# Kernel optimization log

Measured on AMD Instinct MI355X. Metric: run time of the kernel, lower is better.

The kernel has to match this reference:

```python
import jax, jax.numpy as jnp
import numpy as np

B, N, D = 4, 1024, 1024
NH = 16
HS = D // NH
HID = 4 * D
EPS = 1e-5

def layernorm(x, w, b):
    mu = jnp.mean(x, axis=-1, keepdims=True)
    var = jnp.mean(jnp.square(x - mu), axis=-1, keepdims=True)
    return (x - mu) * jax.lax.rsqrt(var + EPS) * w + b

def setup_inputs() -> dict:
    key = jax.random.key(0)
    ks = jax.random.split(key, 8)
    s = lambda fan_in: 1.0 / np.sqrt(fan_in)
    return {
        "x": jax.random.normal(ks[0], (B, N, D), jnp.float32),
        "qkv_w": jax.random.uniform(ks[1], (3 * D, D), jnp.float32, -s(D), s(D)),
        "proj_w": jax.random.uniform(ks[2], (D, D), jnp.float32, -s(D), s(D)),
        "proj_b": jax.random.uniform(ks[3], (D,), jnp.float32, -s(D), s(D)),
        "ln1_w": jnp.ones((D,), jnp.float32),
        "ln1_b": jnp.zeros((D,), jnp.float32),
        "fc1_w": jax.random.uniform(ks[4], (HID, D), jnp.float32, -s(D), s(D)),
        "fc1_b": jax.random.uniform(ks[5], (HID,), jnp.float32, -s(D), s(D)),
        "fc2_w": jax.random.uniform(ks[6], (D, HID), jnp.float32, -s(HID), s(HID)),
        "fc2_b": jax.random.uniform(ks[7], (D,), jnp.float32, -s(HID), s(HID)),
        "ln2_w": jnp.ones((D,), jnp.float32),
        "ln2_b": jnp.zeros((D,), jnp.float32),
    }

def attention(x, qkv_w, proj_w, proj_b):
    # x: [b, n, d]; qkv linear (no bias), split into q,k,v per head
    qkv = jnp.einsum('bnd,ed->bne', x, qkv_w)              # [b, n, 3d]
    qkv = qkv.reshape(B, N, 3, NH, HS).transpose(2, 0, 3, 1, 4)  # [3, b, nh, n, hs]
    q, k, v = qkv[0], qkv[1], qkv[2]
    scale = HS ** -0.5
    # mask=False => self.mask == 1, so (mask-1)*LARGE_NUMBER == 0
    att = jax.nn.softmax(scale * jnp.einsum('bhqe,bhke->bhqk', q, k), axis=-1)
    y = jnp.einsum('bhqk,bhke->bhqe', att, v)              # [b, nh, n, hs]
    y = y.transpose(0, 2, 1, 3).reshape(B, N, D)
    return jnp.einsum('bnd,ed->bne', y, proj_w) + proj_b

def mlp(x, fc1_w, fc1_b, fc2_w, fc2_b):
    h = jax.nn.gelu(jnp.einsum('bnd,hd->bnh', x, fc1_w) + fc1_b, approximate=False)
    return jnp.einsum('bnh,dh->bnd', h, fc2_w) + fc2_b

def reference(x, qkv_w, proj_w, proj_b, ln1_w, ln1_b, fc1_w, fc1_b, fc2_w, fc2_b, ln2_w, ln2_b):
    x = x + attention(layernorm(x, ln1_w, ln1_b), qkv_w, proj_w, proj_b)
    x = x + mlp(layernorm(x, ln2_w, ln2_b), fc1_w, fc1_b, fc2_w, fc2_b)
    return x
```

## Files before the change

### kernel.cpp

```cpp
#include <hip/hip_runtime.h>
#include <hip/hip_bf16.h>

typedef __attribute__((ext_vector_type(8))) short short8;
typedef __attribute__((ext_vector_type(8))) unsigned short ushort8;
typedef __attribute__((ext_vector_type(4))) float floatx4;

#define DEV static __device__ __forceinline__

DEV unsigned short f2bf(float f) {
  unsigned int u = __builtin_bit_cast(unsigned int, f);
  u += 0x7fff + ((u >> 16) & 1);
  return (unsigned short)(u >> 16);
}
DEV float bf2f(unsigned short u) {
  return __builtin_bit_cast(float, (unsigned int)u << 16);
}
DEV unsigned int cvtpk_bf16(float lo, float hi) {
  unsigned int r;
  asm("v_cvt_pk_bf16_f32 %0, %1, %2" : "=v"(r) : "v"(lo), "v"(hi));
  return r;
}

DEV void gload_lds16(const void* g, void* l) {
  __builtin_amdgcn_global_load_lds(
      (const __attribute__((address_space(1))) unsigned int*)g,
      (__attribute__((address_space(3))) unsigned int*)l, 16, 0, 0);
}

__global__ __launch_bounds__(256) void cvt4_kernel(const float* __restrict__ w0,
                                                   const float* __restrict__ w1,
                                                   const float* __restrict__ w2,
                                                   const float* __restrict__ w3,
                                                   unsigned short* __restrict__ o0,
                                                   unsigned short* __restrict__ o1,
                                                   unsigned short* __restrict__ o2,
                                                   unsigned short* __restrict__ o3) {
  int i = blockIdx.x * 256 + threadIdx.x;
  const float* in; unsigned short* out; int j;
  if (i < 786432)       { in = w0; out = o0; j = i; }
  else if (i < 1048576) { in = w1; out = o1; j = i - 786432; }
  else if (i < 2097152) { in = w2; out = o2; j = i - 1048576; }
  else                  { in = w3; out = o3; j = i - 2097152; }
  float4 v = reinterpret_cast<const float4*>(in)[j];
  ushort4 o;
  o.x = f2bf(v.x); o.y = f2bf(v.y); o.z = f2bf(v.z); o.w = f2bf(v.w);
  reinterpret_cast<ushort4*>(out)[j] = o;
}

__global__ __launch_bounds__(256) void ln_kernel(const float* __restrict__ x,
                                                 const float* __restrict__ w,
                                                 const float* __restrict__ b,
                                                 unsigned short* __restrict__ out) {
  const int row = blockIdx.x;
  const float* xr = x + (size_t)row * 1024;
  float4 v = reinterpret_cast<const float4*>(xr)[threadIdx.x];
  float s  = v.x + v.y + v.z + v.w;
  float ss = v.x*v.x + v.y*v.y + v.z*v.z + v.w*v.w;
  #pragma unroll
  for (int off = 1; off < 64; off <<= 1) {
    s  += __shfl_xor(s, off);
    ss += __shfl_xor(ss, off);
  }
  __shared__ float red[8];
  const int wid = threadIdx.x >> 6, lane = threadIdx.x & 63;
  if (lane == 0) { red[wid] = s; red[4 + wid] = ss; }
  __syncthreads();
  s  = red[0] + red[1] + red[2] + red[3];
  ss = red[4] + red[5] + red[6] + red[7];
  const float mu  = s * (1.0f / 1024.0f);
  const float var = ss * (1.0f / 1024.0f) - mu * mu;
  const float rstd = rsqrtf(var + 1e-5f);
  float4 wv = reinterpret_cast<const float4*>(w)[threadIdx.x];
  float4 bv = reinterpret_cast<const float4*>(b)[threadIdx.x];
  ushort4 o;
  o.x = f2bf((v.x - mu) * rstd * wv.x + bv.x);
  o.y = f2bf((v.y - mu) * rstd * wv.y + bv.y);
  o.z = f2bf((v.z - mu) * rstd * wv.z + bv.z);
  o.w = f2bf((v.w - mu) * rstd * wv.w + bv.w);
  reinterpret_cast<ushort4*>(out)[(size_t)row * 256 + threadIdx.x] = o;
}

template<int EPI>
__global__ __launch_bounds__(512, 2) void gemm256(const unsigned short* __restrict__ A,
                                                  const unsigned short* __restrict__ Bw,
                                                  unsigned short* __restrict__ outb,
                                                  const float* __restrict__ bias,
                                                  int K, int N, int NT) {
  __shared__ unsigned short As[2][256 * 64];
  __shared__ unsigned short Bs[2][256 * 64];
  const int tid = threadIdx.x, lane = tid & 63, wid = tid >> 6;
  const int wr = wid >> 2, wc = wid & 3;
  const int fr = lane & 15, s0 = lane >> 4;

  const int nwg = gridDim.x;
  const int qq = nwg >> 3, rr8 = nwg & 7, xcd = blockIdx.x & 7, lid = blockIdx.x >> 3;
  const int wg = (xcd < rr8 ? xcd * (qq + 1) : rr8 * (qq + 1) + (xcd - rr8) * qq) + lid;
  const int brow = (wg / NT) * 256, bcol = (wg % NT) * 256;

  const unsigned short* ag[4];
  const unsigned short* bg[4];
  #pragma unroll
  for (int L = 0; L < 4; L++) {
    const int idx = L * 512 + tid;
    const int row = idx >> 3;
    const int ss  = ((idx & 7) ^ (row & 7)) * 8;
    ag[L] = A  + (size_t)(brow + row) * K + ss;
    bg[L] = Bw + (size_t)(bcol + row) * K + ss;
  }
  const int ldst = tid * 8;

  #define STG256(kt, buf)                                                     \
    do {                                                                      \
      const int ko = (kt) * 64;                                               \
      gload_lds16(ag[0] + ko, &As[buf][ldst]);                                \
      gload_lds16(ag[1] + ko, &As[buf][4096 + ldst]);                         \
      gload_lds16(ag[2] + ko, &As[buf][8192 + ldst]);                         \
      gload_lds16(ag[3] + ko, &As[buf][12288 + ldst]);                        \
      gload_lds16(bg[0] + ko, &Bs[buf][ldst]);                                \
      gload_lds16(bg[1] + ko, &Bs[buf][4096 + ldst]);                         \
      gload_lds16(bg[2] + ko, &Bs[buf][8192 + ldst]);                         \
      gload_lds16(bg[3] + ko, &Bs[buf][12288 + ldst]);                        \
    } while (0)

  const int xs = fr & 7;
  const int aoff = (wr * 128 + fr) * 64;
  const int boff = (wc * 64 + fr) * 64;
  const int sl0 = ((0 + s0) ^ xs) * 8;
  const int sl1 = ((4 + s0) ^ xs) * 8;

  floatx4 acc[8][4];
  #pragma unroll
  for (int m = 0; m < 8; m++)
    #pragma unroll
    for (int n = 0; n < 4; n++) acc[m][n] = (floatx4){0.f, 0.f, 0.f, 0.f};

  const int NTK = K >> 6;
  STG256(0, 0);

  for (int kt = 0; kt < NTK; ++kt) {
    const int cur = kt & 1;
    asm volatile("s_waitcnt vmcnt(0)" ::: "memory");
    __builtin_amdgcn_s_barrier();
    if (kt + 1 < NTK) STG256(kt + 1, cur ^ 1);

    const unsigned short* Ac = As[cur];
    const unsigned short* Bc = Bs[cur];
    short8 bfv[4][2], a0[4][2], a1[4][2];

    #pragma unroll
    for (int n = 0; n < 4; n++) {
      bfv[n][0] = *reinterpret_cast<const short8*>(Bc + boff + n * 1024 + sl0);
      bfv[n][1] = *reinterpret_cast<const short8*>(Bc + boff + n * 1024 + sl1);
    }
    #pragma unroll
    for (int m = 0; m < 4; m++) {
      a0[m][0] = *reinterpret_cast<const short8*>(Ac + aoff + m * 1024 + sl0);
      a0[m][1] = *reinterpret_cast<const short8*>(Ac + aoff + m * 1024 + sl1);
    }
    __builtin_amdgcn_s_setprio(1);
    #pragma unroll
    for (int m = 0; m < 4; m++)
      #pragma unroll
      for (int n = 0; n < 4; n++) {
        acc[m][n] = __builtin_amdgcn_mfma_f32_16x16x32_bf16(a0[m][0], bfv[n][0], acc[m][n], 0, 0, 0);
        acc[m][n] = __builtin_amdgcn_mfma_f32_16x16x32_bf16(a0[m][1], bfv[n][1], acc[m][n], 0, 0, 0);
      }
    __builtin_amdgcn_s_setprio(0);
    #pragma unroll
    for (int m = 0; m < 4; m++) {
      a1[m][0] = *reinterpret_cast<const short8*>(Ac + aoff + (m + 4) * 1024 + sl0);
      a1[m][1] = *reinterpret_cast<const short8*>(Ac + aoff + (m + 4) * 1024 + sl1);
    }
    __builtin_amdgcn_s_setprio(1);
    #pragma unroll
    for (int m = 0; m < 4; m++)
      #pragma unroll
      for (int n = 0; n < 4; n++) {
        acc[m + 4][n] = __builtin_amdgcn_mfma_f32_16x16x32_bf16(a1[m][0], bfv[n][0], acc[m + 4][n], 0, 0, 0);
        acc[m + 4][n] = __builtin_amdgcn_mfma_f32_16x16x32_bf16(a1[m][1], bfv[n][1], acc[m + 4][n], 0, 0, 0);
      }
    __builtin_amdgcn_s_setprio(0);
  }
  #undef STG256

  #pragma unroll
  for (int m = 0; m < 8; m++) {
    #pragma unroll
    for (int n = 0; n < 4; n++) {
      const int col = bcol + wc * 64 + n * 16 + fr;
      #pragma unroll
      for (int r = 0; r < 4; r++) {
        const size_t idx = (size_t)(brow + wr * 128 + m * 16 + s0 * 4 + r) * N + col;
        float v = acc[m][n][r];
        if (EPI == 1) {
          v += bias[col];
          const float u = v * 0.7978845608f * (1.0f + 0.044715f * v * v);
          const float e = __expf(2.0f * u);
          v = v * (e / (e + 1.0f));
        }
        outb[idx] = f2bf(v);
      }
    }
  }
}

__global__ __launch_bounds__(512) void gemm128sk(const unsigned short* __restrict__ A,
                                                 const unsigned short* __restrict__ Bw,
                                                 unsigned short* __restrict__ outb,
                                                 int K, int Ksl, int N, int NT, int ntiles) {
  __shared__ unsigned short As[4][128 * 32];
  __shared__ unsigned short Bs[4][128 * 32];
  const int tid = threadIdx.x, lane = tid & 63, wid = tid >> 6;
  const int wrow = (wid >> 2) * 64, wcol = (wid & 3) * 32;
  const int fr = lane & 15, s0 = lane >> 4;

  const int nwg = gridDim.x;
  const int qq = nwg >> 3, rr8 = nwg & 7, xcd = blockIdx.x & 7, lid = blockIdx.x >> 3;
  const int wg = (xcd < rr8 ? xcd * (qq + 1) : rr8 * (qq + 1) + (xcd - rr8) * qq) + lid;
  const int kslice = wg / ntiles, t = wg % ntiles;
  const int brow = (t / NT) * 128, bcol = (t % NT) * 128;
  const int kofs = kslice * Ksl;

  const int srow = tid >> 2;
  const int sslot = ((tid & 3) ^ ((srow >> 1) & 3)) * 8;
  const unsigned short* ag = A  + (size_t)(brow + srow) * K + kofs + sslot;
  const unsigned short* bg = Bw + (size_t)(bcol + srow) * K + kofs + sslot;
  const int ldst = tid * 8;

  #define STG(kt, buf)                              \
    do {                                            \
      const int ko = (kt) * 32;                     \
      gload_lds16(ag + ko, &As[buf][ldst]);         \
      gload_lds16(bg + ko, &Bs[buf][ldst]);         \
    } while (0)

  const int slr = (s0 ^ ((fr >> 1) & 3)) * 8;

  floatx4 acc[4][2];
  #pragma unroll
  for (int i = 0; i < 4; i++)
    #pragma unroll
    for (int j = 0; j < 2; j++) acc[i][j] = (floatx4){0.f, 0.f, 0.f, 0.f};

  const int NTK = Ksl >> 5;
  STG(0, 0);
  STG(1, 1);
  STG(2, 2);

  for (int kt = 0; kt < NTK; ++kt) {
    const int cur = kt & 3;
    if (kt < NTK - 2) {
      asm volatile("s_waitcnt vmcnt(4)" ::: "memory");
    } else if (kt == NTK - 2) {
      asm volatile("s_waitcnt vmcnt(2)" ::: "memory");
    } else {
      asm volatile("s_waitcnt vmcnt(0)" ::: "memory");
    }
    __builtin_amdgcn_s_barrier();
    if (kt + 3 < NTK) STG(kt + 3, (kt + 3) & 3);

    short8 af[4], bf[2];
    #pragma unroll
    for (int i = 0; i < 4; i++)
      af[i] = *reinterpret_cast<const short8*>(&As[cur][(wrow + i * 16 + fr) * 32 + slr]);
    #pragma unroll
    for (int j = 0; j < 2; j++)
      bf[j] = *reinterpret_cast<const short8*>(&Bs[cur][(wcol + j * 16 + fr) * 32 + slr]);
    __builtin_amdgcn_s_setprio(1);
    #pragma unroll
    for (int i = 0; i < 4; i++)
      #pragma unroll
      for (int j = 0; j < 2; j++)
        acc[i][j] = __builtin_amdgcn_mfma_f32_16x16x32_bf16(af[i], bf[j], acc[i][j], 0, 0, 0);
    __builtin_amdgcn_s_setprio(0);
  }
  #undef STG

  unsigned short* po = outb + (size_t)kslice * ((size_t)ntiles * 16384);
  const int erow = brow + wrow + (s0 << 2);
  const int ecol = bcol + wcol + fr;
  #pragma unroll
  for (int i = 0; i < 4; i++)
    #pragma unroll
    for (int j = 0; j < 2; j++)
      #pragma unroll
      for (int r = 0; r < 4; r++)
        po[(size_t)(erow + i * 16 + r) * N + ecol + j * 16] = f2bf(acc[i][j][r]);
}

__global__ __launch_bounds__(256) void red_ln(const unsigned short* __restrict__ p0,
                                              const unsigned short* __restrict__ p1,
                                              const float* __restrict__ x,
                                              const float* __restrict__ bias,
                                              const float* __restrict__ lw,
                                              const float* __restrict__ lb,
                                              float* __restrict__ x1,
                                              unsigned short* __restrict__ xn) {
  const int row = blockIdx.x, t = threadIdx.x;
  const size_t o4 = (size_t)row * 256 + t;
  ushort4 a = reinterpret_cast<const ushort4*>(p0)[o4];
  ushort4 c = reinterpret_cast<const ushort4*>(p1)[o4];
  float4 xv = reinterpret_cast<const float4*>(x)[o4];
  float4 bv = reinterpret_cast<const float4*>(bias)[t];
  float4 v;
  v.x = bf2f(a.x) + bf2f(c.x) + bv.x + xv.x;
  v.y = bf2f(a.y) + bf2f(c.y) + bv.y + xv.y;
  v.z = bf2f(a.z) + bf2f(c.z) + bv.z + xv.z;
  v.w = bf2f(a.w) + bf2f(c.w) + bv.w + xv.w;
  reinterpret_cast<float4*>(x1)[o4] = v;

  float s  = v.x + v.y + v.z + v.w;
  float ss = v.x*v.x + v.y*v.y + v.z*v.z + v.w*v.w;
  #pragma unroll
  for (int off = 1; off < 64; off <<= 1) {
    s  += __shfl_xor(s, off);
    ss += __shfl_xor(ss, off);
  }
  __shared__ float red[8];
  const int wid = t >> 6, lane = t & 63;
  if (lane == 0) { red[wid] = s; red[4 + wid] = ss; }
  __syncthreads();
  s  = red[0] + red[1] + red[2] + red[3];
  ss = red[4] + red[5] + red[6] + red[7];
  const float mu  = s * (1.0f / 1024.0f);
  const float var = ss * (1.0f / 1024.0f) - mu * mu;
  const float rstd = rsqrtf(var + 1e-5f);
  float4 wv = reinterpret_cast<const float4*>(lw)[t];
  float4 lv = reinterpret_cast<const float4*>(lb)[t];
  ushort4 o;
  o.x = f2bf((v.x - mu) * rstd * wv.x + lv.x);
  o.y = f2bf((v.y - mu) * rstd * wv.y + lv.y);
  o.z = f2bf((v.z - mu) * rstd * wv.z + lv.z);
  o.w = f2bf((v.w - mu) * rstd * wv.w + lv.w);
  reinterpret_cast<ushort4*>(xn)[o4] = o;
}

__global__ __launch_bounds__(256) void red_out(const unsigned short* __restrict__ p0,
                                               const unsigned short* __restrict__ p1,
                                               const float* __restrict__ x1,
                                               const float* __restrict__ bias,
                                               float* __restrict__ out) {
  const size_t i4 = (size_t)blockIdx.x * 256 + threadIdx.x;
  const int c4 = (int)(i4 & 255);
  ushort4 a = reinterpret_cast<const ushort4*>(p0)[i4];
  ushort4 c = reinterpret_cast<const ushort4*>(p1)[i4];
  float4 xv = reinterpret_cast<const float4*>(x1)[i4];
  float4 bv = reinterpret_cast<const float4*>(bias)[c4];
  float4 v;
  v.x = bf2f(a.x) + bf2f(c.x) + bv.x + xv.x;
  v.y = bf2f(a.y) + bf2f(c.y) + bv.y + xv.y;
  v.z = bf2f(a.z) + bf2f(c.z) + bv.z + xv.z;
  v.w = bf2f(a.w) + bf2f(c.w) + bv.w + xv.w;
  reinterpret_cast<float4*>(out)[i4] = v;
}

__global__ __launch_bounds__(256) void vtrans_kernel(const unsigned short* __restrict__ qkv,
                                                     unsigned short* __restrict__ vt) {
  __shared__ unsigned short T[64][66];
  const int nt = blockIdx.x, bh = blockIdx.y;
  const int b = bh >> 4, h = bh & 15;
  const unsigned short* src = qkv + (size_t)b * 1024 * 3072 + 2048 + h * 64;
  const int r = threadIdx.x >> 3, s = threadIdx.x & 7;
  ushort8 a0 = *reinterpret_cast<const ushort8*>(src + (size_t)(nt * 64 + r) * 3072 + s * 8);
  ushort8 a1 = *reinterpret_cast<const ushort8*>(src + (size_t)(nt * 64 + r + 32) * 3072 + s * 8);
  #pragma unroll
  for (int j = 0; j < 8; j++) {
    T[r][s * 8 + j]      = a0[j];
    T[r + 32][s * 8 + j] = a1[j];
  }
  __syncthreads();
  ushort8 o0, o1;
  #pragma unroll
  for (int j = 0; j < 8; j++) {
    o0[j] = T[s * 8 + j][r];
    o1[j] = T[s * 8 + j][r + 32];
  }
  unsigned short* dst = vt + (size_t)bh * 64 * 1024 + nt * 64 + s * 8;
  *reinterpret_cast<ushort8*>(dst + (size_t)r * 1024)        = o0;
  *reinterpret_cast<ushort8*>(dst + (size_t)(r + 32) * 1024) = o1;
}

__global__ __launch_bounds__(512) void attn_kernel(const unsigned short* __restrict__ qkv,
                                                   const unsigned short* __restrict__ vt,
                                                   unsigned short* __restrict__ y) {
  __shared__ unsigned short Ks[2][64 * 64];
  __shared__ unsigned short Vs[2][64 * 64];
  __shared__ unsigned long long Pq[8][256];

  const int tid = threadIdx.x;
  const int lane = tid & 63;
  const int w = tid >> 6;
  const int wg = (blockIdx.x & 7) * 64 + (blockIdx.x >> 3);
  const int bh = wg >> 3, qt = wg & 7;
  const int b = bh >> 4, h = bh & 15;
  const int fr = lane & 15, s0 = lane >> 4;
  const int sw = fr & 7;
  const size_t RS = 3072;

  const unsigned short* qbase = qkv + (size_t)b * 1024 * RS + h * 64;
  const unsigned short* kbase = qbase + 1024;
  const unsigned short* vbase = vt + (size_t)bh * 64 * 1024;

  const float SC = 0.125f * 1.44269504089f;

  short8 aq[2];
  {
    const unsigned short* qrow = qbase + (size_t)(qt * 128 + w * 16 + fr) * RS;
    ushort8 q0 = *reinterpret_cast<const ushort8*>(qrow + s0 * 8);
    ushort8 q1 = *reinterpret_cast<const ushort8*>(qrow + 32 + s0 * 8);
    #pragma unroll
    for (int i = 0; i < 8; i++) {
      q0[i] = f2bf(bf2f(q0[i]) * SC);
      q1[i] = f2bf(bf2f(q1[i]) * SC);
    }
    aq[0] = __builtin_bit_cast(short8, q0);
    aq[1] = __builtin_bit_cast(short8, q1);
  }

  float l_run = 0.f;
  floatx4 accy[4];
  #pragma unroll
  for (int d = 0; d < 4; d++) accy[d] = (floatx4){0.f, 0.f, 0.f, 0.f};

  const int krow = tid >> 3, kslot = tid & 7;
  const int gslot = (kslot ^ (krow & 7)) * 8;
  const unsigned short* kg = kbase + (size_t)krow * RS + gslot;
  const unsigned short* vg = vbase + (size_t)krow * 1024 + gslot;

  #define STAGE(t, buf)                                           \
    do {                                                          \
      gload_lds16(kg + (size_t)(t) * 64 * RS, &Ks[buf][tid * 8]); \
      gload_lds16(vg + (size_t)(t) * 64,      &Vs[buf][tid * 8]); \
    } while (0)

  STAGE(0, 0);
  int cur = 0;

  for (int kt = 0; kt < 16; ++kt) {
    asm volatile("s_waitcnt vmcnt(0)" ::: "memory");
    __builtin_amdgcn_s_barrier();
    if (kt < 15) STAGE(kt + 1, cur ^ 1);

    const unsigned short* Kt = Ks[cur];
    const unsigned short* Vc = Vs[cur];

    floatx4 st[4];
    __builtin_amdgcn_s_setprio(1);
    #pragma unroll
    for (int f = 0; f < 4; ++f) {
      const unsigned short* krw = Kt + (f * 16 + fr) * 64;
      short8 kb0 = *reinterpret_cast<const short8*>(krw + (((s0)     ^ sw) << 3));
      short8 kb1 = *reinterpret_cast<const short8*>(krw + (((s0 + 4) ^ sw) << 3));
      floatx4 s = (floatx4){0.f, 0.f, 0.f, 0.f};
      s = __builtin_amdgcn_mfma_f32_16x16x32_bf16(kb0, aq[0], s, 0, 0, 0);
      s = __builtin_amdgcn_mfma_f32_16x16x32_bf16(kb1, aq[1], s, 0, 0, 0);
      st[f] = s;
    }
    __builtin_amdgcn_s_setprio(0);

    float ps = 0.f;
    unsigned long long pk[4];
    #pragma unroll
    for (int f = 0; f < 4; f++) {
      float p0 = exp2f(st[f][0]);
      float p1 = exp2f(st[f][1]);
      float p2 = exp2f(st[f][2]);
      float p3 = exp2f(st[f][3]);
      ps += (p0 + p1) + (p2 + p3);
      unsigned int lo = cvtpk_bf16(p0, p1);
      unsigned int hi = cvtpk_bf16(p2, p3);
      pk[f] = (unsigned long long)lo | ((unsigned long long)hi << 32);
    }
    ps += __shfl_xor(ps, 16);
    ps += __shfl_xor(ps, 32);
    l_run += ps;

    #pragma unroll
    for (int f = 0; f < 4; f++)
      Pq[w][(f * 4 + s0) * 16 + (fr ^ (s0 << 2))] = pk[f];

    __builtin_amdgcn_s_setprio(1);
    #pragma unroll
    for (int ks = 0; ks < 2; ++ks) {
      const int b0 = ks * 8 + s0 * 2, b1 = b0 + 1;
      unsigned long long q0 = Pq[w][b0 * 16 + (fr ^ ((b0 & 3) << 2))];
      unsigned long long q1 = Pq[w][b1 * 16 + (fr ^ ((b1 & 3) << 2))];
      ulonglong2 u; u.x = q0; u.y = q1;
      short8 ap = __builtin_bit_cast(short8, u);
      const int sA = ((ks * 4 + s0) ^ sw) << 3;
      #pragma unroll
      for (int j = 0; j < 4; ++j) {
        short8 vb = *reinterpret_cast<const short8*>(Vc + (j * 16 + fr) * 64 + sA);
        accy[j] = __builtin_amdgcn_mfma_f32_16x16x32_bf16(ap, vb, accy[j], 0, 0, 0);
      }
    }
    __builtin_amdgcn_s_setprio(0);
    cur ^= 1;
  }
  #undef STAGE

  float linv[4];
  #pragma unroll
  for (int r = 0; r < 4; r++) linv[r] = 1.0f / __shfl(l_run, s0 * 4 + r);
  #pragma unroll
  for (int r = 0; r < 4; r++) {
    const size_t grow2 =
        (size_t)(b * 1024 + qt * 128 + w * 16 + s0 * 4 + r) * 1024 + h * 64;
    #pragma unroll
    for (int j = 0; j < 4; ++j)
      y[grow2 + j * 16 + fr] = f2bf(accy[j][r] * linv[r]);
  }
}

extern "C" void kernel_launch(void* const* d_in, const int* in_sizes, int n_in,
                              void* d_out, int out_size, void* d_ws, size_t ws_size,
                              hipStream_t stream) {
  const float* x      = (const float*)d_in[0];
  const float* qkv_w  = (const float*)d_in[1];
  const float* proj_w = (const float*)d_in[2];
  const float* proj_b = (const float*)d_in[3];
  const float* ln1_w  = (const float*)d_in[4];
  const float* ln1_b  = (const float*)d_in[5];
  const float* fc1_w  = (const float*)d_in[6];
  const float* fc1_b  = (const float*)d_in[7];
  const float* fc2_w  = (const float*)d_in[8];
  const float* fc2_b  = (const float*)d_in[9];
  const float* ln2_w  = (const float*)d_in[10];
  const float* ln2_b  = (const float*)d_in[11];
  float* out = (float*)d_out;

  char* ws = (char*)d_ws;
  unsigned short* qkvw16  = (unsigned short*)(ws + 0);
  unsigned short* projw16 = (unsigned short*)(ws + 6291456);
  unsigned short* fc1w16  = (unsigned short*)(ws + 8388608);
  unsigned short* fc2w16  = (unsigned short*)(ws + 16777216);
  float*          x1      = (float*)(ws + 25165824);
  unsigned short* vt      = (unsigned short*)(ws + 25165824);
  unsigned short* xn      = (unsigned short*)(ws + 41943040);
  unsigned short* big     = (unsigned short*)(ws + 50331648);
  unsigned short* pp      = big;
  unsigned short* fp      = (unsigned short*)(ws + 0);

  cvt4_kernel<<<12288, 256, 0, stream>>>(qkv_w, proj_w, fc1_w, fc2_w,
                                         qkvw16, projw16, fc1w16, fc2w16);

  ln_kernel<<<4096, 256, 0, stream>>>(x, ln1_w, ln1_b, xn);
  gemm128sk<<<768, 512, 0, stream>>>(xn, qkvw16, big, 1024, 1024, 3072, 24, 768);
  vtrans_kernel<<<dim3(16, 64), 256, 0, stream>>>(big, vt);
  attn_kernel<<<512, 512, 0, stream>>>(big, vt, xn);
  gemm128sk<<<512, 512, 0, stream>>>(xn, projw16, pp, 1024, 512, 1024, 8, 256);
  red_ln<<<4096, 256, 0, stream>>>(pp, pp + 4194304, x, proj_b, ln2_w, ln2_b, x1, xn);
  gemm256<1><<<256, 512, 0, stream>>>(xn, fc1w16, big, fc1_b, 1024, 4096, 16);
  gemm128sk<<<512, 512, 0, stream>>>(big, fc2w16, fp, 4096, 2048, 1024, 8, 256);
  red_out<<<4096, 256, 0, stream>>>(fp, fp + 4194304, x1, fc2_b, out);
}
```

Baseline: 227.0 us.

## Use templated BK=32 GEMM with higher occupancy for QKV and FC1

Replaces the 256x256 BK=64 GEMM with a templated BM x 256 kernel using BK=32 tiles and a new swizzle, halving LDS use so four workgroups can fit per CU (launch bounds 512,4). The FC1 GEMM uses the new kernel with BM=256, and the QKV projection moves off the split-K 128 GEMM onto a 128x256 tile variant. The aim is more occupancy and better latency hiding, at the cost of more barriers per K and less reuse per LDS load.

```diff
diff --git a/kernel.cpp b/kernel.cpp
--- a/kernel.cpp
+++ b/kernel.cpp
@@ -80,14 +80,16 @@
   reinterpret_cast<ushort4*>(out)[(size_t)row * 256 + threadIdx.x] = o;
 }
 
-template<int EPI>
-__global__ __launch_bounds__(512, 2) void gemm256(const unsigned short* __restrict__ A,
-                                                  const unsigned short* __restrict__ Bw,
-                                                  unsigned short* __restrict__ outb,
-                                                  const float* __restrict__ bias,
-                                                  int K, int N, int NT) {
-  __shared__ unsigned short As[2][256 * 64];
-  __shared__ unsigned short Bs[2][256 * 64];
+template<int EPI, int BM>
+__global__ __launch_bounds__(512, 4) void gemmbk32(const unsigned short* __restrict__ A,
+                                                   const unsigned short* __restrict__ Bw,
+                                                   unsigned short* __restrict__ outb,
+                                                   const float* __restrict__ bias,
+                                                   int K, int N, int NT) {
+  constexpr int ALOADS = BM / 128;
+  constexpr int MREP   = BM / 32;
+  __shared__ unsigned short As[2][BM * 32];
+  __shared__ unsigned short Bs[2][256 * 32];
   const int tid = threadIdx.x, lane = tid & 63, wid = tid >> 6;
   const int wr = wid >> 2, wc = wid & 3;
   const int fr = lane & 15, s0 = lane >> 4;
@@ -95,102 +97,83 @@
   const int nwg = gridDim.x;
   const int qq = nwg >> 3, rr8 = nwg & 7, xcd = blockIdx.x & 7, lid = blockIdx.x >> 3;
   const int wg = (xcd < rr8 ? xcd * (qq + 1) : rr8 * (qq + 1) + (xcd - rr8) * qq) + lid;
-  const int brow = (wg / NT) * 256, bcol = (wg % NT) * 256;
-
-  const unsigned short* ag[4];
-  const unsigned short* bg[4];
-  #pragma unroll
-  for (int L = 0; L < 4; L++) {
+  const int brow = (wg / NT) * BM, bcol = (wg % NT) * 256;
+
+  const unsigned short* ag[ALOADS];
+  const unsigned short* bg[2];
+  #pragma unroll
+  for (int L = 0; L < ALOADS; L++) {
     const int idx = L * 512 + tid;
-    const int row = idx >> 3;
-    const int ss  = ((idx & 7) ^ (row & 7)) * 8;
-    ag[L] = A  + (size_t)(brow + row) * K + ss;
+    const int row = idx >> 2;
+    const int ss  = ((idx & 3) ^ ((row >> 1) & 3)) * 8;
+    ag[L] = A + (size_t)(brow + row) * K + ss;
+  }
+  #pragma unroll
+  for (int L = 0; L < 2; L++) {
+    const int idx = L * 512 + tid;
+    const int row = idx >> 2;
+    const int ss  = ((idx & 3) ^ ((row >> 1) & 3)) * 8;
     bg[L] = Bw + (size_t)(bcol + row) * K + ss;
   }
   const int ldst = tid * 8;
 
-  #define STG256(kt, buf)                                                     \
-    do {                                                                      \
-      const int ko = (kt) * 64;                                               \
-      gload_lds16(ag[0] + ko, &As[buf][ldst]);                                \
-      gload_lds16(ag[1] + ko, &As[buf][4096 + ldst]);                         \
-      gload_lds16(ag[2] + ko, &As[buf][8192 + ldst]);                         \
-      gload_lds16(ag[3] + ko, &As[buf][12288 + ldst]);                        \
-      gload_lds16(bg[0] + ko, &Bs[buf][ldst]);                                \
-      gload_lds16(bg[1] + ko, &Bs[buf][4096 + ldst]);                         \
-      gload_lds16(bg[2] + ko, &Bs[buf][8192 + ldst]);                         \
-      gload_lds16(bg[3] + ko, &Bs[buf][12288 + ldst]);                        \
+  #define STG32(kt, buf)                                          \
+    do {                                                          \
+      const int ko = (kt) * 32;                                   \
+      _Pragma("unroll")                                           \
+      for (int L = 0; L < ALOADS; L++)                            \
+        gload_lds16(ag[L] + ko, &As[buf][L * 4096 + ldst]);       \
+      _Pragma("unroll")                                           \
+      for (int L = 0; L < 2; L++)                                 \
+        gload_lds16(bg[L] + ko, &Bs[buf][L * 4096 + ldst]);       \
     } while (0)
 
-  const int xs = fr & 7;
-  const int aoff = (wr * 128 + fr) * 64;
-  const int boff = (wc * 64 + fr) * 64;
-  const int sl0 = ((0 + s0) ^ xs) * 8;
-  const int sl1 = ((4 + s0) ^ xs) * 8;
-
-  floatx4 acc[8][4];
-  #pragma unroll
-  for (int m = 0; m < 8; m++)
+  const int slr = (s0 ^ ((fr >> 1) & 3)) * 8;
+  const int aoff = (wr * (BM / 2) + fr) * 32;
+  const int boff = (wc * 64 + fr) * 32;
+
+  floatx4 acc[MREP][4];
+  #pragma unroll
+  for (int m = 0; m < MREP; m++)
     #pragma unroll
     for (int n = 0; n < 4; n++) acc[m][n] = (floatx4){0.f, 0.f, 0.f, 0.f};
 
-  const int NTK = K >> 6;
-  STG256(0, 0);
+  const int NTK = K >> 5;
+  STG32(0, 0);
 
   for (int kt = 0; kt < NTK; ++kt) {
     const int cur = kt & 1;
     asm volatile("s_waitcnt vmcnt(0)" ::: "memory");
     __builtin_amdgcn_s_barrier();
-    if (kt + 1 < NTK) STG256(kt + 1, cur ^ 1);
+    if (kt + 1 < NTK) STG32(kt + 1, cur ^ 1);
 
     const unsigned short* Ac = As[cur];
     const unsigned short* Bc = Bs[cur];
-    short8 bfv[4][2], a0[4][2], a1[4][2];
-
-    #pragma unroll
-    for (int n = 0; n < 4; n++) {
-      bfv[n][0] = *reinterpret_cast<const short8*>(Bc + boff + n * 1024 + sl0);
-      bfv[n][1] = *reinterpret_cast<const short8*>(Bc + boff + n * 1024 + sl1);
-    }
-    #pragma unroll
-    for (int m = 0; m < 4; m++) {
-      a0[m][0] = *reinterpret_cast<const short8*>(Ac + aoff + m * 1024 + sl0);
-      a0[m][1] = *reinterpret_cast<const short8*>(Ac + aoff + m * 1024 + sl1);
-    }
+    short8 af[MREP], bf[4];
+    #pragma unroll
+    for (int n = 0; n < 4; n++)
+      bf[n] = *reinterpret_cast<const short8*>(Bc + boff + n * 512 + slr);
+    #pragma unroll
+    for (int m = 0; m < MREP; m++)
+      af[m] = *reinterpret_cast<const short8*>(Ac + aoff + m * 512 + slr);
     __builtin_amdgcn_s_setprio(1);
     #pragma unroll
-    for (int m = 0; m < 4; m++)
+    for (int m = 0; m < MREP; m++)
       #pragma unroll
-      for (int n = 0; n < 4; n++) {
-        acc[m][n] = __builtin_amdgcn_mfma_f32_16x16x32_bf16(a0[m][0], bfv[n][0], acc[m][n], 0, 0, 0);
-        acc[m][n] = __builtin_amdgcn_mfma_f32_16x16x32_bf16(a0[m][1], bfv[n][1], acc[m][n], 0, 0, 0);
-      }
+      for (int n = 0; n < 4; n++)
+        acc[m][n] = __builtin_amdgcn_mfma_f32_16x16x32_bf16(af[m], bf[n], acc[m][n], 0, 0, 0);
     __builtin_amdgcn_s_setprio(0);
-    #pragma unroll
-    for (int m = 0; m < 4; m++) {
-      a1[m][0] = *reinterpret_cast<const short8*>(Ac + aoff + (m + 4) * 1024 + sl0);
-      a1[m][1] = *reinterpret_cast<const short8*>(Ac + aoff + (m + 4) * 1024 + sl1);
-    }
-    __builtin_amdgcn_s_setprio(1);
-    #pragma unroll
-    for (int m = 0; m < 4; m++)
-      #pragma unroll
-      for (int n = 0; n < 4; n++) {
-        acc[m + 4][n] = __builtin_amdgcn_mfma_f32_16x16x32_bf16(a1[m][0], bfv[n][0], acc[m + 4][n], 0, 0, 0);
-        acc[m + 4][n] = __builtin_amdgcn_mfma_f32_16x16x32_bf16(a1[m][1], bfv[n][1], acc[m + 4][n], 0, 0, 0);
-      }
-    __builtin_amdgcn_s_setprio(0);
-  }
-  #undef STG256
-
-  #pragma unroll
-  for (int m = 0; m < 8; m++) {
+  }
+  #undef STG32
+
+  #pragma unroll
+  for (int m = 0; m < MREP; m++) {
     #pragma unroll
     for (int n = 0; n < 4; n++) {
       const int col = bcol + wc * 64 + n * 16 + fr;
       #pragma unroll
       for (int r = 0; r < 4; r++) {
-        const size_t idx = (size_t)(brow + wr * 128 + m * 16 + s0 * 4 + r) * N + col;
+        const size_t idx = (size_t)(brow + wr * (BM / 2) + m * 16 + s0 * 4 + r) * N + col;
         float v = acc[m][n][r];
         if (EPI == 1) {
           v += bias[col];
@@ -545,12 +528,12 @@
                                          qkvw16, projw16, fc1w16, fc2w16);
 
   ln_kernel<<<4096, 256, 0, stream>>>(x, ln1_w, ln1_b, xn);
-  gemm128sk<<<768, 512, 0, stream>>>(xn, qkvw16, big, 1024, 1024, 3072, 24, 768);
+  gemmbk32<0, 128><<<384, 512, 0, stream>>>(xn, qkvw16, big, nullptr, 1024, 3072, 12);
   vtrans_kernel<<<dim3(16, 64), 256, 0, stream>>>(big, vt);
   attn_kernel<<<512, 512, 0, stream>>>(big, vt, xn);
   gemm128sk<<<512, 512, 0, stream>>>(xn, projw16, pp, 1024, 512, 1024, 8, 256);
   red_ln<<<4096, 256, 0, stream>>>(pp, pp + 4194304, x, proj_b, ln2_w, ln2_b, x1, xn);
-  gemm256<1><<<256, 512, 0, stream>>>(xn, fc1w16, big, fc1_b, 1024, 4096, 16);
+  gemmbk32<1, 256><<<256, 512, 0, stream>>>(xn, fc1w16, big, fc1_b, 1024, 4096, 16);
   gemm128sk<<<512, 512, 0, stream>>>(big, fc2w16, fp, 4096, 2048, 1024, 8, 256);
   red_out<<<4096, 256, 0, stream>>>(fp, fp + 4194304, x1, fc2_b, out);
 }
```

Result: slower. 494.2 us (+117.7%).
